# Performance work log

Hardware: AMD Instinct MI355X
Metric: run time of the kernel (lower is better)

The kernel has to match this reference:

```python
import jax, jax.numpy as jnp
import numpy as np

NEG_MAX = -jnp.finfo(jnp.float32).max


def apply_rotary(x):
    # x: (b, h, n, d) with d = key_dim; interleaved rotary (lucidrains rotary-embedding-torch)
    d = x.shape[-1]
    n = x.shape[-2]
    inv_freq = 1.0 / (10000.0 ** (jnp.arange(0, d, 2, dtype=jnp.float32) / d))
    t = jnp.arange(n, dtype=jnp.float32)
    freqs = t[:, None] * inv_freq[None, :]              # (n, d/2)
    cos, sin = jnp.cos(freqs), jnp.sin(freqs)
    x1, x2 = x[..., 0::2], x[..., 1::2]                 # even/odd interleaved pairs
    out1 = x1 * cos - x2 * sin
    out2 = x1 * sin + x2 * cos
    return jnp.stack([out1, out2], axis=-1).reshape(x.shape)


def setup_inputs() -> dict:
    key = jax.random.key(0)
    ks = jax.random.split(key, 12)
    b, n, dim, de = 2, 1024, 256, 64
    h, kd, vd = 8, 32, 32
    node_in = jax.random.normal(ks[0], (b, n, dim), dtype=jnp.float32)
    edge_in = jax.random.normal(ks[1], (b, n, n, de), dtype=jnp.float32)
    mask = jax.random.randint(ks[2], (b, n), 0, 2).astype(bool)
    s = 1.0 / np.sqrt(dim)
    Wq = jax.random.normal(ks[3], (dim, h * kd), dtype=jnp.float32) * s
    Wk = jax.random.normal(ks[4], (dim, h * kd), dtype=jnp.float32) * s
    Wv = jax.random.normal(ks[5], (dim, h * vd), dtype=jnp.float32) * s
    We = jax.random.normal(ks[6], (de, h), dtype=jnp.float32) * (1.0 / np.sqrt(de))
    be = jax.random.normal(ks[7], (h,), dtype=jnp.float32) * 0.01
    Wo = jax.random.normal(ks[8], (h * (vd + de), dim), dtype=jnp.float32) * (1.0 / np.sqrt(h * (vd + de)))
    bo = jax.random.normal(ks[9], (dim,), dtype=jnp.float32) * 0.01
    return {"node_in": node_in, "edge_in": edge_in, "mask": mask,
            "Wq": Wq, "Wk": Wk, "Wv": Wv, "We": We, "be": be, "Wo": Wo, "bo": bo}


def reference(node_in, edge_in, mask, Wq, Wk, Wv, We, be, Wo, bo):
    b, n, dim = node_in.shape
    h = be.shape[0]
    kd = Wq.shape[1] // h
    vd = Wv.shape[1] // h
    num_attn_logits = 2
    node_scale = (num_attn_logits * kd) ** -0.5
    edge_scale = num_attn_logits ** -0.5

    # projections -> (b, h, n, d)
    def proj(W, d):
        return (node_in @ W).reshape(b, n, h, d).transpose(0, 2, 1, 3)
    q, k, v = proj(Wq, kd), proj(Wk, kd), proj(Wv, vd)
    q, k = apply_rotary(q), apply_rotary(k)

    logits = jnp.einsum('bhid,bhjd->bhij', q, k) * node_scale
    edge_bias = (jnp.einsum('bijd,dh->bijh', edge_in, We) + be)  # (b, n, n, h)
    logits = logits + edge_bias.transpose(0, 3, 1, 2) * edge_scale

    pair_mask = mask[:, :, None] & mask[:, None, :]              # (b, n, n)
    logits = jnp.where(pair_mask[:, None, :, :], logits, NEG_MAX)

    attn = jax.nn.softmax(logits, axis=-1)                       # (b, h, n, n)

    res_node = jnp.einsum('bhij,bhjd->bhid', attn, v)            # (b, h, n, vd)
    res_edge = jnp.einsum('bhij,bijd->bhid', attn, edge_in)      # (b, h, n, de)

    res_node = res_node.transpose(0, 2, 1, 3).reshape(b, n, h * vd)
    res_edge = res_edge.transpose(0, 2, 1, 3).reshape(b, n, -1)
    out = jnp.concatenate([res_node, res_edge], axis=-1) @ Wo + bo
    return out
```

## Files before the change

### kernel.cpp

```cpp
#include <hip/hip_runtime.h>
#include <hip/hip_bf16.h>

typedef float f32x4 __attribute__((ext_vector_type(4)));
typedef short short8 __attribute__((ext_vector_type(8)));
typedef unsigned short u16;
typedef unsigned int u32;
typedef unsigned int u32x4 __attribute__((ext_vector_type(4)));
typedef unsigned short u16x8 __attribute__((ext_vector_type(8)));

#define NEG_MAX (-3.4028234663852886e38f)
#define NODE_SCALE 0.125f
#define EDGE_SCALE 0.70710678118654752f
#define ESTR 72

__device__ __forceinline__ float bf2f(u16 u) {
  unsigned int w = ((unsigned int)u) << 16;
  return __builtin_bit_cast(float, w);
}
__device__ __forceinline__ u16 f2bf(float f) {
  unsigned int x = __builtin_bit_cast(unsigned int, f);
  x = x + 0x7FFFu + ((x >> 16) & 1u);
  return (u16)(x >> 16);
}
__device__ __forceinline__ float asf(u32 x) { return __builtin_bit_cast(float, x); }
__device__ __forceinline__ u32 cvtpk(float lo, float hi) {
  u32 r;
  asm("v_cvt_pk_bf16_f32 %0, %1, %2" : "=v"(r) : "v"(lo), "v"(hi));
  return r;
}

__global__ void mask_norm(const unsigned char* __restrict__ mraw,
                          float* __restrict__ mask_f) {
  __shared__ int flags;
  int t = threadIdx.x;
  if (t == 0) flags = 0;
  __syncthreads();
  const unsigned int* mu = (const unsigned int*)mraw;
  int f = 0;
  for (int e = t; e < 512; e += 256) { if (mu[e] > 1u) f |= 1; }
  for (int e = t; e < 2048; e += 256) { if (mraw[e] > 1) f |= 2; }
  if (f) atomicOr(&flags, f);
  __syncthreads();
  int fl = flags;
  for (int e = t; e < 2048; e += 256) {
    float v;
    if (!(fl & 1))      v = (mu[e] != 0u) ? 1.f : 0.f;
    else if (!(fl & 2)) v = (mraw[e] != 0) ? 1.f : 0.f;
    else                v = (((const float*)mraw)[e] != 0.f) ? 1.f : 0.f;
    mask_f[e] = v;
  }
}

__global__ __launch_bounds__(256) void qkv_rope(
    const float* __restrict__ node, const float* __restrict__ Wq,
    const float* __restrict__ Wk, const float* __restrict__ Wv,
    float* __restrict__ qw, u16* __restrict__ kwb, u16* __restrict__ vwb) {
  __shared__ __align__(16) float xs[8 * 256];
  int t = threadIdx.x;
  int row0 = blockIdx.x * 8;
#pragma unroll
  for (int p = 0; p < 2; ++p) {
    int f = p * 256 + t;
    *(f32x4*)(&xs[f * 4]) = *(const f32x4*)(node + (size_t)row0 * 256 + f * 4);
  }
  __syncthreads();
  float qa[8], ka[8], va[8];
#pragma unroll
  for (int r = 0; r < 8; ++r) { qa[r] = 0.f; ka[r] = 0.f; va[r] = 0.f; }
  for (int c = 0; c < 256; ++c) {
    float wq = Wq[c * 256 + t];
    float wk = Wk[c * 256 + t];
    float wv = Wv[c * 256 + t];
#pragma unroll
    for (int r = 0; r < 8; ++r) {
      float x = xs[r * 256 + c];
      qa[r] += x * wq; ka[r] += x * wk; va[r] += x * wv;
    }
  }
  int d = t & 31;
  float inv = powf(10000.f, -((float)(2 * (d >> 1)) * (1.f / 32.f)));
  int h = t >> 5;
#pragma unroll
  for (int r = 0; r < 8; ++r) {
    int gr = row0 + r;
    int b = gr >> 10, i = gr & 1023;
    float ang = (float)i * inv;
    float sn, cs;
    sincosf(ang, &sn, &cs);
    float qp = __shfl_xor(qa[r], 1, 64);
    float kp = __shfl_xor(ka[r], 1, 64);
    float qo = (d & 1) ? (qp * sn + qa[r] * cs) : (qa[r] * cs - qp * sn);
    float ko = (d & 1) ? (kp * sn + ka[r] * cs) : (ka[r] * cs - kp * sn);
    int idx = ((b * 8 + h) * 1024 + i) * 32 + d;
    qw[idx] = qo;
    kwb[idx] = f2bf(ko);
    vwb[idx] = f2bf(va[r]);
  }
}

__global__ __launch_bounds__(256) void attn_fused(
    const float* __restrict__ edge, const float* __restrict__ qw,
    const u16* __restrict__ kwb, const u16* __restrict__ vwb,
    const float* __restrict__ We, const float* __restrict__ be,
    const float* __restrict__ mask_f, float* __restrict__ rescat) {
  __shared__ __align__(16) u16 Ew[4][16 * ESTR];
  __shared__ __align__(16) float Bg[4][8][20];
  __shared__ __align__(16) float Pg[4][8][20];
  __shared__ float Rg[4][8];
  __shared__ __align__(16) float MRG[4][1040];

  int bid = blockIdx.x;
  int xcd = bid & 7, slot = bid >> 3;
  int b = xcd >> 2;
  int i = (xcd & 3) * 256 + slot;
  int t = threadIdx.x;
  int lane = t & 63;
  int w = __builtin_amdgcn_readfirstlane(t >> 6);

  int hg = lane >> 4, jl = lane & 15;
  int hD = lane >> 3, sD = lane & 7;
  int jrl = lane >> 2, c4 = lane & 3;
  int jh = sD >> 2, do4 = sD & 3;

  float mi = mask_f[b * 1024 + i];
  u32 mb = 0;
  if (mi != 0.f) {
#pragma unroll
    for (int tt = 0; tt < 16; ++tt) {
      float v = mask_f[b * 1024 + tt * 64 + w * 16 + jl];
      mb |= (v != 0.f ? 1u : 0u) << tt;
    }
  }
  float bes1 = be[hg] * EDGE_SCALE, bes2 = be[hg + 4] * EDGE_SCALE;

  u32 qp1[16], qp2[16];
  {
    const float* q1 = qw + ((size_t)((b * 8 + hg) * 1024 + i)) * 32;
    const float* q2 = qw + ((size_t)((b * 8 + hg + 4) * 1024 + i)) * 32;
#pragma unroll
    for (int e = 0; e < 16; ++e) {
      qp1[e] = (u32)f2bf(q1[2 * e]) | ((u32)f2bf(q1[2 * e + 1]) << 16);
      qp2[e] = (u32)f2bf(q2[2 * e]) | ((u32)f2bf(q2[2 * e + 1]) << 16);
    }
  }

  short8 weA0, weA1;
  {
    int hh = lane & 15, g = lane >> 4;
#pragma unroll
    for (int e = 0; e < 8; ++e) {
      int d0 = g * 8 + e;
      float w0 = (hh < 8) ? We[d0 * 8 + hh] * EDGE_SCALE : 0.f;
      float w1 = (hh < 8) ? We[(d0 + 32) * 8 + hh] * EDGE_SCALE : 0.f;
      weA0[e] = (short)f2bf(w0);
      weA1[e] = (short)f2bf(w1);
    }
  }

  const float* ebase = edge + ((size_t)(b * 1024 + i)) * (1024 * 64);
  const float* gsrc = ebase + (size_t)(w * 16 + jrl) * 64 + c4 * 16;
  u16* ewbase = &Ew[w][0];
  int wa0 = jrl * ESTR + (((c4 * 2 + 0) + 3 * jrl) & 7) * 8;
  int wa1 = jrl * ESTR + (((c4 * 2 + 1) + 3 * jrl) & 7) * 8;
  int ra0 = jl * ESTR + (((hg + 0) + 3 * jl) & 7) * 8;
  int ra1 = jl * ESTR + (((hg + 4) + 3 * jl) & 7) * 8;

  {
    f32x4 a0 = __builtin_nontemporal_load((const f32x4*)(gsrc + 0));
    f32x4 a1 = __builtin_nontemporal_load((const f32x4*)(gsrc + 4));
    f32x4 a2 = __builtin_nontemporal_load((const f32x4*)(gsrc + 8));
    f32x4 a3 = __builtin_nontemporal_load((const f32x4*)(gsrc + 12));
    u32x4 w0, w1;
    w0[0] = cvtpk(a0.x, a0.y); w0[1] = cvtpk(a0.z, a0.w);
    w0[2] = cvtpk(a1.x, a1.y); w0[3] = cvtpk(a1.z, a1.w);
    w1[0] = cvtpk(a2.x, a2.y); w1[1] = cvtpk(a2.z, a2.w);
    w1[2] = cvtpk(a3.x, a3.y); w1[3] = cvtpk(a3.z, a3.w);
    *(u32x4*)(ewbase + wa0) = w0;
    *(u32x4*)(ewbase + wa1) = w1;
  }

  float m1 = NEG_MAX, m2 = NEG_MAX, s1 = 0.f, s2 = 0.f;
  f32x4 av0 = {0.f, 0.f, 0.f, 0.f}, av1 = {0.f, 0.f, 0.f, 0.f};
  f32x4 ae0 = {0.f, 0.f, 0.f, 0.f}, ae1 = {0.f, 0.f, 0.f, 0.f};

  for (int tt = 0; tt < 16; ++tt) {
    int j0 = tt * 64;
    bool pf = tt < 15;
    f32x4 st0, st1, st2, st3;
    if (pf) {
      const float* g = gsrc + (size_t)(j0 + 64) * 64;
      st0 = __builtin_nontemporal_load((const f32x4*)(g + 0));
      st1 = __builtin_nontemporal_load((const f32x4*)(g + 4));
      st2 = __builtin_nontemporal_load((const f32x4*)(g + 8));
      st3 = __builtin_nontemporal_load((const f32x4*)(g + 12));
    }
    int jg = j0 + w * 16 + jl;
    const u16* kr1 = kwb + ((size_t)((b * 8 + hg) * 1024 + jg)) * 32;
    const u16* kr2 = kwb + ((size_t)((b * 8 + hg + 4) * 1024 + jg)) * 32;
    u32x4 k1[4], k2[4];
#pragma unroll
    for (int g = 0; g < 4; ++g) {
      k1[g] = *(const u32x4*)(kr1 + g * 8);
      k2[g] = *(const u32x4*)(kr2 + g * 8);
    }
    {
      short8 bf0 = *(const short8*)(ewbase + ra0);
      short8 bf1 = *(const short8*)(ewbase + ra1);
      f32x4 bacc = {0.f, 0.f, 0.f, 0.f};
      bacc = __builtin_amdgcn_mfma_f32_16x16x32_bf16(weA0, bf0, bacc, 0, 0, 0);
      bacc = __builtin_amdgcn_mfma_f32_16x16x32_bf16(weA1, bf1, bacc, 0, 0, 0);
      if (lane < 32) {
        Bg[w][hg * 4 + 0][jl] = bacc[0];
        Bg[w][hg * 4 + 1][jl] = bacc[1];
        Bg[w][hg * 4 + 2][jl] = bacc[2];
        Bg[w][hg * 4 + 3][jl] = bacc[3];
      }
    }
    float qk1 = 0.f, qk2 = 0.f;
#pragma unroll
    for (int g = 0; g < 4; ++g)
#pragma unroll
      for (int e = 0; e < 4; ++e) {
        u32 ka = k1[g][e], qa = qp1[g * 4 + e];
        qk1 = fmaf(asf(ka << 16), asf(qa << 16), qk1);
        qk1 = fmaf(asf(ka & 0xffff0000u), asf(qa & 0xffff0000u), qk1);
        u32 kb = k2[g][e], qb = qp2[g * 4 + e];
        qk2 = fmaf(asf(kb << 16), asf(qb << 16), qk2);
        qk2 = fmaf(asf(kb & 0xffff0000u), asf(qb & 0xffff0000u), qk2);
      }
    {
      float bias1 = Bg[w][hg][jl], bias2 = Bg[w][hg + 4][jl];
      bool pm = (mb >> tt) & 1u;
      float l1 = pm ? (NODE_SCALE * qk1 + bias1 + bes1) : NEG_MAX;
      float l2 = pm ? (NODE_SCALE * qk2 + bias2 + bes2) : NEG_MAX;
      float mx1 = l1, mx2 = l2;
#pragma unroll
      for (int off = 1; off < 16; off <<= 1) {
        mx1 = fmaxf(mx1, __shfl_xor(mx1, off, 64));
        mx2 = fmaxf(mx2, __shfl_xor(mx2, off, 64));
      }
      float mn1 = fmaxf(m1, mx1), mn2 = fmaxf(m2, mx2);
      float p1 = __expf(l1 - mn1), p2 = __expf(l2 - mn2);
      float ps1 = p1, ps2 = p2;
#pragma unroll
      for (int off = 1; off < 16; off <<= 1) {
        ps1 += __shfl_xor(ps1, off, 64);
        ps2 += __shfl_xor(ps2, off, 64);
      }
      float r1 = __expf(m1 - mn1), r2 = __expf(m2 - mn2);
      s1 = s1 * r1 + ps1; m1 = mn1;
      s2 = s2 * r2 + ps2; m2 = mn2;
      Pg[w][hg][jl] = p1;
      Pg[w][hg + 4][jl] = p2;
      if (jl == 0) { Rg[w][hg] = r1; Rg[w][hg + 4] = r2; }
    }
    {
      float r = Rg[w][hD];
      f32x4 pr0 = *(const f32x4*)&Pg[w][hD][0];
      f32x4 pr1 = *(const f32x4*)&Pg[w][hD][4];
      f32x4 pr2 = *(const f32x4*)&Pg[w][hD][8];
      f32x4 pr3 = *(const f32x4*)&Pg[w][hD][12];
      {
        const u16* vb = vwb + ((size_t)((b * 8 + hD) * 1024 + j0 + w * 16 + jh * 8)) * 32 + do4 * 8;
        f32x4 prA = jh ? pr2 : pr0, prB = jh ? pr3 : pr1;
        f32x4 sv0 = {0.f, 0.f, 0.f, 0.f}, sv1 = {0.f, 0.f, 0.f, 0.f};
#pragma unroll
        for (int x = 0; x < 8; ++x) {
          float p = (x < 4) ? prA[x] : prB[x - 4];
          u32x4 vv = *(const u32x4*)(vb + (size_t)x * 32);
          f32x4 e0 = {asf(vv[0] << 16), asf(vv[0] & 0xffff0000u),
                      asf(vv[1] << 16), asf(vv[1] & 0xffff0000u)};
          f32x4 e1 = {asf(vv[2] << 16), asf(vv[2] & 0xffff0000u),
                      asf(vv[3] << 16), asf(vv[3] & 0xffff0000u)};
          sv0 += e0 * p;
          sv1 += e1 * p;
        }
        av0 = av0 * r + sv0;
        av1 = av1 * r + sv1;
      }
      {
        f32x4 se0 = {0.f, 0.f, 0.f, 0.f}, se1 = {0.f, 0.f, 0.f, 0.f};
#pragma unroll
        for (int x = 0; x < 16; ++x) {
          float p = (x < 4) ? pr0[x] : (x < 8) ? pr1[x - 4]
                  : (x < 12) ? pr2[x - 8] : pr3[x - 12];
          const u16* ep = ewbase + x * ESTR + ((sD + 3 * x) & 7) * 8;
          u32x4 ee = *(const u32x4*)ep;
          f32x4 e0 = {asf(ee[0] << 16), asf(ee[0] & 0xffff0000u),
                      asf(ee[1] << 16), asf(ee[1] & 0xffff0000u)};
          f32x4 e1 = {asf(ee[2] << 16), asf(ee[2] & 0xffff0000u),
                      asf(ee[3] << 16), asf(ee[3] & 0xffff0000u)};
          se0 += e0 * p;
          se1 += e1 * p;
        }
        ae0 = ae0 * r + se0;
        ae1 = ae1 * r + se1;
      }
    }
    if (pf) {
      u32x4 w0, w1;
      w0[0] = cvtpk(st0.x, st0.y); w0[1] = cvtpk(st0.z, st0.w);
      w0[2] = cvtpk(st1.x, st1.y); w0[3] = cvtpk(st1.z, st1.w);
      w1[0] = cvtpk(st2.x, st2.y); w1[1] = cvtpk(st2.z, st2.w);
      w1[2] = cvtpk(st3.x, st3.y); w1[3] = cvtpk(st3.z, st3.w);
      *(u32x4*)(ewbase + wa0) = w0;
      *(u32x4*)(ewbase + wa1) = w1;
    }
  }

  if (jl == 0) {
    MRG[w][hg] = m1; MRG[w][hg + 4] = m2;
    MRG[w][8 + hg] = s1; MRG[w][8 + hg + 4] = s2;
  }
  *(f32x4*)&MRG[w][16 + jh * 256 + hD * 32 + do4 * 8] = av0;
  *(f32x4*)&MRG[w][16 + jh * 256 + hD * 32 + do4 * 8 + 4] = av1;
  *(f32x4*)&MRG[w][528 + hD * 64 + sD * 8] = ae0;
  *(f32x4*)&MRG[w][528 + hD * 64 + sD * 8 + 4] = ae1;
  __syncthreads();
  {
    int h = t >> 5, d = t & 31;
    float mx = fmaxf(fmaxf(MRG[0][h], MRG[1][h]), fmaxf(MRG[2][h], MRG[3][h]));
    float ew[4];
    float ssum = 0.f, vsum = 0.f;
#pragma unroll
    for (int ww = 0; ww < 4; ++ww) {
      ew[ww] = __expf(MRG[ww][h] - mx);
      ssum += MRG[ww][8 + h] * ew[ww];
      vsum += (MRG[ww][16 + h * 32 + d] + MRG[ww][16 + 256 + h * 32 + d]) * ew[ww];
    }
    float inv = 1.f / ssum;
    size_t obase = ((size_t)(b * 1024 + i)) * 768;
    rescat[obase + h * 32 + d] = vsum * inv;
    float e0 = 0.f, e1 = 0.f;
#pragma unroll
    for (int ww = 0; ww < 4; ++ww) {
      e0 += MRG[ww][528 + h * 64 + d] * ew[ww];
      e1 += MRG[ww][528 + h * 64 + 32 + d] * ew[ww];
    }
    rescat[obase + 256 + h * 64 + d] = e0 * inv;
    rescat[obase + 256 + h * 64 + 32 + d] = e1 * inv;
  }
}

__global__ __launch_bounds__(256) void out_proj(
    const float* __restrict__ rescat, const float* __restrict__ Wo,
    const float* __restrict__ bo, float* __restrict__ out) {
  __shared__ __align__(16) float xs[8 * 768];
  int t = threadIdx.x;
  int row0 = blockIdx.x * 8;
#pragma unroll
  for (int p = 0; p < 6; ++p) {
    int f = p * 256 + t;
    *(f32x4*)(&xs[f * 4]) = *(const f32x4*)(rescat + (size_t)row0 * 768 + f * 4);
  }
  __syncthreads();
  float acc[8];
#pragma unroll
  for (int r = 0; r < 8; ++r) acc[r] = 0.f;
  for (int c = 0; c < 768; ++c) {
    float w = Wo[c * 256 + t];
#pragma unroll
    for (int r = 0; r < 8; ++r) acc[r] += xs[r * 768 + c] * w;
  }
  float bias = bo[t];
#pragma unroll
  for (int r = 0; r < 8; ++r)
    out[(size_t)(row0 + r) * 256 + t] = acc[r] + bias;
}

extern "C" void kernel_launch(void* const* d_in, const int* in_sizes, int n_in,
                              void* d_out, int out_size, void* d_ws, size_t ws_size,
                              hipStream_t stream) {
  const float* node = (const float*)d_in[0];
  const float* edge = (const float*)d_in[1];
  const unsigned char* mask = (const unsigned char*)d_in[2];
  const float* Wq = (const float*)d_in[3];
  const float* Wk = (const float*)d_in[4];
  const float* Wv = (const float*)d_in[5];
  const float* We = (const float*)d_in[6];
  const float* be = (const float*)d_in[7];
  const float* Wo = (const float*)d_in[8];
  const float* bo = (const float*)d_in[9];

  float* ws = (float*)d_ws;
  float* qw = ws;
  u16* kwb = (u16*)(ws + 524288);
  u16* vwb = kwb + 524288;
  float* rescat = ws + 1048576;
  float* mask_f = ws + 2621440;

  hipLaunchKernelGGL(mask_norm, dim3(1), dim3(256), 0, stream, mask, mask_f);
  hipLaunchKernelGGL(qkv_rope, dim3(256), dim3(256), 0, stream,
                     node, Wq, Wk, Wv, qw, kwb, vwb);
  hipLaunchKernelGGL(attn_fused, dim3(2048), dim3(256), 0, stream,
                     edge, qw, kwb, vwb, We, be, mask_f, rescat);
  hipLaunchKernelGGL(out_proj, dim3(256), dim3(256), 0, stream,
                     rescat, Wo, bo, (float*)d_out);
}
```

Before: 405.4 us.

## Stage edge tile in fp32 LDS and keep q in shared memory

The per-wave edge tile is now stored in LDS as fp32 with a padded stride, not as swizzled bf16. Conversion to bf16 happens only when building the MFMA operands for the edge bias, and the edge-weighted accumulation reads fp32 directly without unpacking. The query vectors move from 32 packed registers per thread into LDS, which reduces register pressure, and the shared buffers are merged into one aliased region. In exchange the kernel uses about twice the LDS for the tile and issues more LDS reads in the QK dot product. It also adds an extra __syncthreads before the merge, which the aliasing requires.

```diff
diff --git a/kernel.cpp b/kernel.cpp
--- a/kernel.cpp
+++ b/kernel.cpp
@@ -11,7 +11,8 @@
 #define NEG_MAX (-3.4028234663852886e38f)
 #define NODE_SCALE 0.125f
 #define EDGE_SCALE 0.70710678118654752f
-#define ESTR 72
+#define TSTR 68
+#define QSTR 36
 
 __device__ __forceinline__ float bf2f(u16 u) {
   unsigned int w = ((unsigned int)u) << 16;
@@ -98,16 +99,13 @@
   }
 }
 
+#define WREG 1704
 __global__ __launch_bounds__(256) void attn_fused(
     const float* __restrict__ edge, const float* __restrict__ qw,
     const u16* __restrict__ kwb, const u16* __restrict__ vwb,
     const float* __restrict__ We, const float* __restrict__ be,
     const float* __restrict__ mask_f, float* __restrict__ rescat) {
-  __shared__ __align__(16) u16 Ew[4][16 * ESTR];
-  __shared__ __align__(16) float Bg[4][8][20];
-  __shared__ __align__(16) float Pg[4][8][20];
-  __shared__ float Rg[4][8];
-  __shared__ __align__(16) float MRG[4][1040];
+  __shared__ __align__(16) float S[4 * WREG];
 
   int bid = blockIdx.x;
   int xcd = bid & 7, slot = bid >> 3;
@@ -117,6 +115,12 @@
   int lane = t & 63;
   int w = __builtin_amdgcn_readfirstlane(t >> 6);
 
+  float* tile = S + w * WREG;
+  float* Pf = tile + 1088;
+  float* Bg = Pf + 160;
+  float* qsw = Bg + 160;
+  float* Rg = qsw + 288;
+
   int hg = lane >> 4, jl = lane & 15;
   int hD = lane >> 3, sD = lane & 7;
   int jrl = lane >> 2, c4 = lane & 3;
@@ -133,15 +137,10 @@
   }
   float bes1 = be[hg] * EDGE_SCALE, bes2 = be[hg + 4] * EDGE_SCALE;
 
-  u32 qp1[16], qp2[16];
   {
-    const float* q1 = qw + ((size_t)((b * 8 + hg) * 1024 + i)) * 32;
-    const float* q2 = qw + ((size_t)((b * 8 + hg + 4) * 1024 + i)) * 32;
-#pragma unroll
-    for (int e = 0; e < 16; ++e) {
-      qp1[e] = (u32)f2bf(q1[2 * e]) | ((u32)f2bf(q1[2 * e + 1]) << 16);
-      qp2[e] = (u32)f2bf(q2[2 * e]) | ((u32)f2bf(q2[2 * e + 1]) << 16);
-    }
+    int qh = lane >> 3, qd = (lane & 7) * 4;
+    f32x4 qv = *(const f32x4*)(qw + ((size_t)((b * 8 + qh) * 1024 + i)) * 32 + qd);
+    *(f32x4*)(qsw + qh * QSTR + qd) = qv;
   }
 
   short8 weA0, weA1;
@@ -159,24 +158,17 @@
 
   const float* ebase = edge + ((size_t)(b * 1024 + i)) * (1024 * 64);
   const float* gsrc = ebase + (size_t)(w * 16 + jrl) * 64 + c4 * 16;
-  u16* ewbase = &Ew[w][0];
-  int wa0 = jrl * ESTR + (((c4 * 2 + 0) + 3 * jrl) & 7) * 8;
-  int wa1 = jrl * ESTR + (((c4 * 2 + 1) + 3 * jrl) & 7) * 8;
-  int ra0 = jl * ESTR + (((hg + 0) + 3 * jl) & 7) * 8;
-  int ra1 = jl * ESTR + (((hg + 4) + 3 * jl) & 7) * 8;
+  float* wdst = tile + jrl * TSTR + c4 * 16;
 
   {
     f32x4 a0 = __builtin_nontemporal_load((const f32x4*)(gsrc + 0));
     f32x4 a1 = __builtin_nontemporal_load((const f32x4*)(gsrc + 4));
     f32x4 a2 = __builtin_nontemporal_load((const f32x4*)(gsrc + 8));
     f32x4 a3 = __builtin_nontemporal_load((const f32x4*)(gsrc + 12));
-    u32x4 w0, w1;
-    w0[0] = cvtpk(a0.x, a0.y); w0[1] = cvtpk(a0.z, a0.w);
-    w0[2] = cvtpk(a1.x, a1.y); w0[3] = cvtpk(a1.z, a1.w);
-    w1[0] = cvtpk(a2.x, a2.y); w1[1] = cvtpk(a2.z, a2.w);
-    w1[2] = cvtpk(a3.x, a3.y); w1[3] = cvtpk(a3.z, a3.w);
-    *(u32x4*)(ewbase + wa0) = w0;
-    *(u32x4*)(ewbase + wa1) = w1;
+    *(f32x4*)(wdst + 0) = a0;
+    *(f32x4*)(wdst + 4) = a1;
+    *(f32x4*)(wdst + 8) = a2;
+    *(f32x4*)(wdst + 12) = a3;
   }
 
   float m1 = NEG_MAX, m2 = NEG_MAX, s1 = 0.f, s2 = 0.f;
@@ -204,32 +196,61 @@
       k2[g] = *(const u32x4*)(kr2 + g * 8);
     }
     {
-      short8 bf0 = *(const short8*)(ewbase + ra0);
-      short8 bf1 = *(const short8*)(ewbase + ra1);
+      const float* rp = tile + jl * TSTR + hg * 8;
+      f32x4 ea0 = *(const f32x4*)(rp + 0);
+      f32x4 ea1 = *(const f32x4*)(rp + 4);
+      f32x4 eb0 = *(const f32x4*)(rp + 32);
+      f32x4 eb1 = *(const f32x4*)(rp + 36);
+      u32x4 p0, p1;
+      p0[0] = cvtpk(ea0.x, ea0.y); p0[1] = cvtpk(ea0.z, ea0.w);
+      p0[2] = cvtpk(ea1.x, ea1.y); p0[3] = cvtpk(ea1.z, ea1.w);
+      p1[0] = cvtpk(eb0.x, eb0.y); p1[1] = cvtpk(eb0.z, eb0.w);
+      p1[2] = cvtpk(eb1.x, eb1.y); p1[3] = cvtpk(eb1.z, eb1.w);
+      short8 bf0 = __builtin_bit_cast(short8, p0);
+      short8 bf1 = __builtin_bit_cast(short8, p1);
       f32x4 bacc = {0.f, 0.f, 0.f, 0.f};
       bacc = __builtin_amdgcn_mfma_f32_16x16x32_bf16(weA0, bf0, bacc, 0, 0, 0);
       bacc = __builtin_amdgcn_mfma_f32_16x16x32_bf16(weA1, bf1, bacc, 0, 0, 0);
       if (lane < 32) {
-        Bg[w][hg * 4 + 0][jl] = bacc[0];
-        Bg[w][hg * 4 + 1][jl] = bacc[1];
-        Bg[w][hg * 4 + 2][jl] = bacc[2];
-        Bg[w][hg * 4 + 3][jl] = bacc[3];
+        float* bg = Bg + hg * 80 + jl;
+        bg[0] = bacc[0];
+        bg[20] = bacc[1];
+        bg[40] = bacc[2];
+        bg[60] = bacc[3];
       }
     }
     float qk1 = 0.f, qk2 = 0.f;
-#pragma unroll
-    for (int g = 0; g < 4; ++g)
-#pragma unroll
-      for (int e = 0; e < 4; ++e) {
-        u32 ka = k1[g][e], qa = qp1[g * 4 + e];
-        qk1 = fmaf(asf(ka << 16), asf(qa << 16), qk1);
-        qk1 = fmaf(asf(ka & 0xffff0000u), asf(qa & 0xffff0000u), qk1);
-        u32 kb = k2[g][e], qb = qp2[g * 4 + e];
-        qk2 = fmaf(asf(kb << 16), asf(qb << 16), qk2);
-        qk2 = fmaf(asf(kb & 0xffff0000u), asf(qb & 0xffff0000u), qk2);
-      }
     {
-      float bias1 = Bg[w][hg][jl], bias2 = Bg[w][hg + 4][jl];
+      const float* q1p = qsw + hg * QSTR;
+      const float* q2p = qsw + (hg + 4) * QSTR;
+#pragma unroll
+      for (int g = 0; g < 4; ++g) {
+        f32x4 q1a = *(const f32x4*)(q1p + g * 8);
+        f32x4 q1b = *(const f32x4*)(q1p + g * 8 + 4);
+        f32x4 q2a = *(const f32x4*)(q2p + g * 8);
+        f32x4 q2b = *(const f32x4*)(q2p + g * 8 + 4);
+        u32 ka0 = k1[g][0], ka1 = k1[g][1], ka2 = k1[g][2], ka3 = k1[g][3];
+        u32 kb0 = k2[g][0], kb1 = k2[g][1], kb2 = k2[g][2], kb3 = k2[g][3];
+        qk1 = fmaf(asf(ka0 << 16), q1a.x, qk1);
+        qk1 = fmaf(asf(ka0 & 0xffff0000u), q1a.y, qk1);
+        qk1 = fmaf(asf(ka1 << 16), q1a.z, qk1);
+        qk1 = fmaf(asf(ka1 & 0xffff0000u), q1a.w, qk1);
+        qk1 = fmaf(asf(ka2 << 16), q1b.x, qk1);
+        qk1 = fmaf(asf(ka2 & 0xffff0000u), q1b.y, qk1);
+        qk1 = fmaf(asf(ka3 << 16), q1b.z, qk1);
+        qk1 = fmaf(asf(ka3 & 0xffff0000u), q1b.w, qk1);
+        qk2 = fmaf(asf(kb0 << 16), q2a.x, qk2);
+        qk2 = fmaf(asf(kb0 & 0xffff0000u), q2a.y, qk2);
+        qk2 = fmaf(asf(kb1 << 16), q2a.z, qk2);
+        qk2 = fmaf(asf(kb1 & 0xffff0000u), q2a.w, qk2);
+        qk2 = fmaf(asf(kb2 << 16), q2b.x, qk2);
+        qk2 = fmaf(asf(kb2 & 0xffff0000u), q2b.y, qk2);
+        qk2 = fmaf(asf(kb3 << 16), q2b.z, qk2);
+        qk2 = fmaf(asf(kb3 & 0xffff0000u), q2b.w, qk2);
+      }
+    }
+    {
+      float bias1 = Bg[hg * 20 + jl], bias2 = Bg[(hg + 4) * 20 + jl];
       bool pm = (mb >> tt) & 1u;
       float l1 = pm ? (NODE_SCALE * qk1 + bias1 + bes1) : NEG_MAX;
       float l2 = pm ? (NODE_SCALE * qk2 + bias2 + bes2) : NEG_MAX;
@@ -250,16 +271,17 @@
       float r1 = __expf(m1 - mn1), r2 = __expf(m2 - mn2);
       s1 = s1 * r1 + ps1; m1 = mn1;
       s2 = s2 * r2 + ps2; m2 = mn2;
-      Pg[w][hg][jl] = p1;
-      Pg[w][hg + 4][jl] = p2;
-      if (jl == 0) { Rg[w][hg] = r1; Rg[w][hg + 4] = r2; }
+      Pf[hg * 20 + jl] = p1;
+      Pf[(hg + 4) * 20 + jl] = p2;
+      if (jl == 0) { Rg[hg] = r1; Rg[hg + 4] = r2; }
     }
     {
-      float r = Rg[w][hD];
-      f32x4 pr0 = *(const f32x4*)&Pg[w][hD][0];
-      f32x4 pr1 = *(const f32x4*)&Pg[w][hD][4];
-      f32x4 pr2 = *(const f32x4*)&Pg[w][hD][8];
-      f32x4 pr3 = *(const f32x4*)&Pg[w][hD][12];
+      float r = Rg[hD];
+      const float* prow = Pf + hD * 20;
+      f32x4 pr0 = *(const f32x4*)(prow + 0);
+      f32x4 pr1 = *(const f32x4*)(prow + 4);
+      f32x4 pr2 = *(const f32x4*)(prow + 8);
+      f32x4 pr3 = *(const f32x4*)(prow + 12);
       {
         const u16* vb = vwb + ((size_t)((b * 8 + hD) * 1024 + j0 + w * 16 + jh * 8)) * 32 + do4 * 8;
         f32x4 prA = jh ? pr2 : pr0, prB = jh ? pr3 : pr1;
@@ -279,17 +301,14 @@
         av1 = av1 * r + sv1;
       }
       {
+        const float* eB = tile + sD * 8;
         f32x4 se0 = {0.f, 0.f, 0.f, 0.f}, se1 = {0.f, 0.f, 0.f, 0.f};
 #pragma unroll
         for (int x = 0; x < 16; ++x) {
           float p = (x < 4) ? pr0[x] : (x < 8) ? pr1[x - 4]
                   : (x < 12) ? pr2[x - 8] : pr3[x - 12];
-          const u16* ep = ewbase + x * ESTR + ((sD + 3 * x) & 7) * 8;
-          u32x4 ee = *(const u32x4*)ep;
-          f32x4 e0 = {asf(ee[0] << 16), asf(ee[0] & 0xffff0000u),
-                      asf(ee[1] << 16), asf(ee[1] & 0xffff0000u)};
-          f32x4 e1 = {asf(ee[2] << 16), asf(ee[2] & 0xffff0000u),
-                      asf(ee[3] << 16), asf(ee[3] & 0xffff0000u)};
+          f32x4 e0 = *(const f32x4*)(eB + x * TSTR);
+          f32x4 e1 = *(const f32x4*)(eB + x * TSTR + 4);
           se0 += e0 * p;
           se1 += e1 * p;
         }
@@ -298,35 +317,35 @@
       }
     }
     if (pf) {
-      u32x4 w0, w1;
-      w0[0] = cvtpk(st0.x, st0.y); w0[1] = cvtpk(st0.z, st0.w);
-      w0[2] = cvtpk(st1.x, st1.y); w0[3] = cvtpk(st1.z, st1.w);
-      w1[0] = cvtpk(st2.x, st2.y); w1[1] = cvtpk(st2.z, st2.w);
-      w1[2] = cvtpk(st3.x, st3.y); w1[3] = cvtpk(st3.z, st3.w);
-      *(u32x4*)(ewbase + wa0) = w0;
-      *(u32x4*)(ewbase + wa1) = w1;
-    }
-  }
-
+      *(f32x4*)(wdst + 0) = st0;
+      *(f32x4*)(wdst + 4) = st1;
+      *(f32x4*)(wdst + 8) = st2;
+      *(f32x4*)(wdst + 12) = st3;
+    }
+  }
+
+  __syncthreads();
+  float* mrg = S + w * 1040;
   if (jl == 0) {
-    MRG[w][hg] = m1; MRG[w][hg + 4] = m2;
-    MRG[w][8 + hg] = s1; MRG[w][8 + hg + 4] = s2;
-  }
-  *(f32x4*)&MRG[w][16 + jh * 256 + hD * 32 + do4 * 8] = av0;
-  *(f32x4*)&MRG[w][16 + jh * 256 + hD * 32 + do4 * 8 + 4] = av1;
-  *(f32x4*)&MRG[w][528 + hD * 64 + sD * 8] = ae0;
-  *(f32x4*)&MRG[w][528 + hD * 64 + sD * 8 + 4] = ae1;
+    mrg[hg] = m1; mrg[hg + 4] = m2;
+    mrg[8 + hg] = s1; mrg[8 + hg + 4] = s2;
+  }
+  *(f32x4*)(mrg + 16 + jh * 256 + hD * 32 + do4 * 8) = av0;
+  *(f32x4*)(mrg + 16 + jh * 256 + hD * 32 + do4 * 8 + 4) = av1;
+  *(f32x4*)(mrg + 528 + hD * 64 + sD * 8) = ae0;
+  *(f32x4*)(mrg + 528 + hD * 64 + sD * 8 + 4) = ae1;
   __syncthreads();
   {
     int h = t >> 5, d = t & 31;
-    float mx = fmaxf(fmaxf(MRG[0][h], MRG[1][h]), fmaxf(MRG[2][h], MRG[3][h]));
+    float mx = fmaxf(fmaxf(S[h], S[1040 + h]), fmaxf(S[2080 + h], S[3120 + h]));
     float ew[4];
     float ssum = 0.f, vsum = 0.f;
 #pragma unroll
     for (int ww = 0; ww < 4; ++ww) {
-      ew[ww] = __expf(MRG[ww][h] - mx);
-      ssum += MRG[ww][8 + h] * ew[ww];
-      vsum += (MRG[ww][16 + h * 32 + d] + MRG[ww][16 + 256 + h * 32 + d]) * ew[ww];
+      const float* mw = S + ww * 1040;
+      ew[ww] = __expf(mw[h] - mx);
+      ssum += mw[8 + h] * ew[ww];
+      vsum += (mw[16 + h * 32 + d] + mw[16 + 256 + h * 32 + d]) * ew[ww];
     }
     float inv = 1.f / ssum;
     size_t obase = ((size_t)(b * 1024 + i)) * 768;
@@ -334,8 +353,9 @@
     float e0 = 0.f, e1 = 0.f;
 #pragma unroll
     for (int ww = 0; ww < 4; ++ww) {
-      e0 += MRG[ww][528 + h * 64 + d] * ew[ww];
-      e1 += MRG[ww][528 + h * 64 + 32 + d] * ew[ww];
+      const float* mw = S + ww * 1040;
+      e0 += mw[528 + h * 64 + d] * ew[ww];
+      e1 += mw[528 + h * 64 + 32 + d] * ew[ww];
     }
     rescat[obase + 256 + h * 64 + d] = e0 * inv;
     rescat[obase + 256 + h * 64 + 32 + d] = e1 * inv;
```

After: 395.5 us. -2.5%, faster.
